# Kernel optimization log

Measured on AMD Instinct MI355X. Metric: run time of the kernel, lower is better.

## Reference

```python
import jax, jax.numpy as jnp
import numpy as np


def setup_inputs() -> dict:
    key = jax.random.key(0)
    x = jax.random.normal(key, (8192, 4096), dtype=jnp.float32)
    return {"x": x, "k": 1}


def reference(x, k):
    # torch.linalg.svdvals returns singular values in descending order;
    # jnp.linalg.svd with compute_uv=False does the same.
    s = jnp.linalg.svd(x, compute_uv=False)  # [min(m, n)], descending
    return jnp.sum(s[:k] ** 2)
```

## Files before the change

kernel.cpp:

```cpp
#include <hip/hip_runtime.h>
#include <hip/hip_fp16.h>
#include <math.h>


#define NROWS 8192
#define NCOLS 4096
#define T_STEPS 16
#define BMV_BLOCKS 512
#define RPC 8

__global__ __launch_bounds__(256) void init_kernel(float* __restrict__ ws) {
    int i = blockIdx.x * 256 + threadIdx.x;
    float* r1 = ws;
    float* r0 = ws + 4096;
    float* slots = ws + 12288;
    unsigned h = (unsigned)i * 2654435761u;
    h ^= h >> 16; h *= 2246822519u; h ^= h >> 13;
    r1[i] = (h & 1u) ? 0.015625f : -0.015625f;
    r0[i] = 0.f;
    if (i < 128) slots[i] = (i == 64 || i == 65) ? 1.f : 0.f;
}

__global__ __launch_bounds__(256) void convert_kernel(const float* __restrict__ A,
                                                      __half* __restrict__ Ah) {
    const float4* A4 = (const float4*)A;
    float2* O2 = (float2*)Ah;
    for (int i = blockIdx.x * 256 + threadIdx.x; i < (NROWS * NCOLS / 4); i += 2048 * 256) {
        float4 f = A4[i];
        union { float2 f2; __half2 h2[2]; } u;
        u.h2[0] = __halves2half2(__float2half_rn(f.x), __float2half_rn(f.y));
        u.h2[1] = __halves2half2(__float2half_rn(f.z), __float2half_rn(f.w));
        O2[i] = u.f2;
    }
}

__device__ __forceinline__ void up8(const float4& p, float* f) {
    const __half2* h = (const __half2*)&p;
    float2 t0 = __half22float2(h[0]);
    float2 t1 = __half22float2(h[1]);
    float2 t2 = __half22float2(h[2]);
    float2 t3 = __half22float2(h[3]);
    f[0] = t0.x; f[1] = t0.y; f[2] = t1.x; f[3] = t1.y;
    f[4] = t2.x; f[5] = t2.y; f[6] = t3.x; f[7] = t3.y;
}

__global__ __launch_bounds__(256, 4) void bmv(const __half* __restrict__ Ah,
                                              const float* __restrict__ rc,
                                              float* __restrict__ partials,
                                              float* __restrict__ slots,
                                              int j) {
    __shared__ float s_lds[RPC];
    int tid = threadIdx.x, lane = tid & 63;
    float inv = rsqrtf(fmaxf(slots[64 + j], 1e-30f));
    int cA = tid * 8, cB = 2048 + tid * 8;
    float vA[8], vB[8];
    {
        const float4* r4 = (const float4*)(rc + cA);
        float4 x = r4[0], y = r4[1];
        vA[0] = x.x * inv; vA[1] = x.y * inv; vA[2] = x.z * inv; vA[3] = x.w * inv;
        vA[4] = y.x * inv; vA[5] = y.y * inv; vA[6] = y.z * inv; vA[7] = y.w * inv;
        const float4* s4 = (const float4*)(rc + cB);
        float4 z = s4[0], w = s4[1];
        vB[0] = z.x * inv; vB[1] = z.y * inv; vB[2] = z.z * inv; vB[3] = z.w * inv;
        vB[4] = w.x * inv; vB[5] = w.y * inv; vB[6] = w.z * inv; vB[7] = w.w * inv;
    }
    float wacc[16];
#pragma unroll
    for (int i = 0; i < 16; ++i) wacc[i] = 0.f;

#pragma unroll 1
    for (int ch = 0; ch < 2; ++ch) {
        int row0 = ch * 4096 + blockIdx.x * RPC;
        const __half* base = Ah + (size_t)row0 * NCOLS;
        float4 alo[RPC], ahi[RPC];
#pragma unroll
        for (int r = 0; r < RPC; ++r) {
            alo[r] = *(const float4*)(base + (size_t)r * NCOLS + cA);
            ahi[r] = *(const float4*)(base + (size_t)r * NCOLS + cB);
        }
        __syncthreads();
        if (tid < RPC) s_lds[tid] = 0.f;
        __syncthreads();
#pragma unroll
        for (int r = 0; r < RPC; ++r) {
            float f[8];
            up8(alo[r], f);
            float sp = f[0] * vA[0] + f[1] * vA[1] + f[2] * vA[2] + f[3] * vA[3]
                     + f[4] * vA[4] + f[5] * vA[5] + f[6] * vA[6] + f[7] * vA[7];
            up8(ahi[r], f);
            sp += f[0] * vB[0] + f[1] * vB[1] + f[2] * vB[2] + f[3] * vB[3]
                + f[4] * vB[4] + f[5] * vB[5] + f[6] * vB[6] + f[7] * vB[7];
#pragma unroll
            for (int off = 32; off > 0; off >>= 1) sp += __shfl_xor(sp, off);
            if (lane == 0) atomicAdd(&s_lds[r], sp);
        }
        __syncthreads();
        if (tid == 0) {
            float aa = 0.f;
#pragma unroll
            for (int r = 0; r < RPC; ++r) aa += s_lds[r] * s_lds[r];
            atomicAdd(&slots[j], aa);
        }
#pragma unroll
        for (int r = 0; r < RPC; ++r) {
            float s = s_lds[r];
            float f[8];
            up8(alo[r], f);
            wacc[0] += s * f[0]; wacc[1] += s * f[1]; wacc[2] += s * f[2]; wacc[3] += s * f[3];
            wacc[4] += s * f[4]; wacc[5] += s * f[5]; wacc[6] += s * f[6]; wacc[7] += s * f[7];
            up8(ahi[r], f);
            wacc[8] += s * f[0]; wacc[9] += s * f[1]; wacc[10] += s * f[2]; wacc[11] += s * f[3];
            wacc[12] += s * f[4]; wacc[13] += s * f[5]; wacc[14] += s * f[6]; wacc[15] += s * f[7];
        }
    }
    float* pb = partials + (size_t)blockIdx.x * NCOLS;
    float4* pa = (float4*)(pb + cA);
    pa[0] = make_float4(wacc[0], wacc[1], wacc[2], wacc[3]);
    pa[1] = make_float4(wacc[4], wacc[5], wacc[6], wacc[7]);
    float4* pc = (float4*)(pb + cB);
    pc[0] = make_float4(wacc[8], wacc[9], wacc[10], wacc[11]);
    pc[1] = make_float4(wacc[12], wacc[13], wacc[14], wacc[15]);
}

__global__ __launch_bounds__(256) void red1(const float* __restrict__ partials,
                                            float* __restrict__ p2) {
    int cb = blockIdx.x >> 5, g = blockIdx.x & 31;
    int col = cb * 256 + threadIdx.x;
    const float* p = partials + (size_t)(g * 16) * NCOLS + col;
    float s = 0.f;
#pragma unroll
    for (int k = 0; k < 16; ++k) s += p[(size_t)k * NCOLS];
    p2[(size_t)g * NCOLS + col] = s;
}

__global__ __launch_bounds__(256) void red2(const float* __restrict__ p2,
                                            float* __restrict__ wt,
                                            const float* __restrict__ rc,
                                            const float* __restrict__ rp,
                                            float* __restrict__ slots,
                                            int j) {
    int tid = threadIdx.x;
    int col = blockIdx.x * 256 + tid;
    float w = 0.f;
#pragma unroll
    for (int g = 0; g < 32; ++g) w += p2[(size_t)g * NCOLS + col];
    float a = slots[j];
    float n2j = fmaxf(slots[64 + j], 1e-30f);
    float n2m = fmaxf(slots[64 + j - 1], 1e-30f);
    float invj = rsqrtf(n2j);
    float cb = sqrtf(n2j / n2m);
    float rn = w - a * invj * rc[col] - cb * rp[col];
    wt[col] = rn;
    float p = rn * rn;
#pragma unroll
    for (int off = 32; off > 0; off >>= 1) p += __shfl_xor(p, off);
    __shared__ float part[4];
    int lane = tid & 63, wq = tid >> 6;
    if (lane == 0) part[wq] = p;
    __syncthreads();
    if (tid == 0)
        atomicAdd(&slots[64 + j + 1], part[0] + part[1] + part[2] + part[3]);
}

__global__ void solve_kernel(const float* __restrict__ slots,
                             float* __restrict__ out, int t) {
    __shared__ float d_s[64], e2_s[64];
    int lane = threadIdx.x;
    d_s[lane] = (lane < t) ? slots[1 + lane] : 0.f;
    e2_s[lane] = (lane < t - 1) ? slots[64 + lane + 2] : 0.f;
    __syncthreads();
    float e_here = sqrtf(e2_s[lane]);
    float e_prev = (lane > 0) ? sqrtf(e2_s[lane - 1]) : 0.f;
    float d = d_s[lane];
    float gersh = (lane < t) ? d + e_here + e_prev : 0.f;
    float dmax = (lane < t) ? d : 0.f;
#pragma unroll
    for (int off = 32; off > 0; off >>= 1) {
        gersh = fmaxf(gersh, __shfl_xor(gersh, off));
        dmax = fmaxf(dmax, __shfl_xor(dmax, off));
    }
    float lo = dmax, hi = gersh + 1e-3f;
    for (int round = 0; round < 3; ++round) {
        float stepw = (hi - lo) * (1.f / 64.f);
        float x = lo + stepw * (lane + 1);
        double qv = 1.0;
        int cnt = 0;
        for (int i = 0; i < t; ++i) {
            double qi = (double)d_s[i] - (double)x - ((i > 0) ? (double)e2_s[i - 1] / qv : 0.0);
            if (fabs(qi) < 1e-300) qi = -1e-300;
            cnt += (qi < 0.0);
            qv = qi;
        }
        unsigned long long m = __ballot(cnt < t);
        if (m) {
            int h = 63 - __clzll(m);
            lo = lo + stepw * (h + 1);
            hi = lo + stepw;
        } else {
            hi = lo + stepw;
        }
    }
    if (lane == 0) out[0] = 0.5f * (lo + hi);
}

extern "C" void kernel_launch(void* const* d_in, const int* in_sizes, int n_in,
                              void* d_out, int out_size, void* d_ws, size_t ws_size,
                              hipStream_t stream) {
    const float* A = (const float*)d_in[0];
    float* out = (float*)d_out;
    float* ws = (float*)d_ws;
    float* vb[3] = {ws, ws + 4096, ws + 8192};
    float* slots = ws + 12288;
    float* p2 = ws + 16384;
    float* partials = ws + 262144;
    __half* Ah = (__half*)((char*)d_ws + (size_t)16 * 1024 * 1024);

    init_kernel<<<16, 256, 0, stream>>>(ws);
    convert_kernel<<<2048, 256, 0, stream>>>(A, Ah);

    const int T = T_STEPS;
    for (int j = 1; j <= T; ++j) {
        float* rc = vb[j % 3];
        float* rp = vb[(j + 2) % 3];
        float* wt = vb[(j + 1) % 3];
        bmv<<<BMV_BLOCKS, 256, 0, stream>>>(Ah, rc, partials, slots, j);
        if (j < T) {
            red1<<<512, 256, 0, stream>>>(partials, p2);
            red2<<<16, 256, 0, stream>>>(p2, wt, rc, rp, slots, j);
        }
    }
    solve_kernel<<<1, 64, 0, stream>>>(slots, out, T);
}
```

Baseline: 848.4 us.

## Fuse Lanczos iterations into one persistent kernel with grid barriers

Replaces the init, convert, per-step matvec, two reduction kernels and the solve kernel with a single persistent kernel of 256 blocks. Stages are separated by atomic-counter grid barriers, and the two-level partial reduction becomes a single in-block reduction per column slice. The goal is to remove dozens of kernel launches and the intermediate reduction buffer. In exchange, it relies on all blocks being co-resident and runs with fewer blocks per matvec. The initial vector placement also changes: the random start vector now sits in the buffer the first step reads.

After: 1.483 ms. 74.8% more time.

```diff
diff --git a/kernel.cpp b/kernel.cpp
--- a/kernel.cpp
+++ b/kernel.cpp
@@ -6,32 +6,25 @@
 #define NROWS 8192
 #define NCOLS 4096
 #define T_STEPS 16
-#define BMV_BLOCKS 512
+#define NBLK 256
 #define RPC 8
-
-__global__ __launch_bounds__(256) void init_kernel(float* __restrict__ ws) {
-    int i = blockIdx.x * 256 + threadIdx.x;
-    float* r1 = ws;
-    float* r0 = ws + 4096;
-    float* slots = ws + 12288;
-    unsigned h = (unsigned)i * 2654435761u;
-    h ^= h >> 16; h *= 2246822519u; h ^= h >> 13;
-    r1[i] = (h & 1u) ? 0.015625f : -0.015625f;
-    r0[i] = 0.f;
-    if (i < 128) slots[i] = (i == 64 || i == 65) ? 1.f : 0.f;
-}
-
-__global__ __launch_bounds__(256) void convert_kernel(const float* __restrict__ A,
-                                                      __half* __restrict__ Ah) {
-    const float4* A4 = (const float4*)A;
-    float2* O2 = (float2*)Ah;
-    for (int i = blockIdx.x * 256 + threadIdx.x; i < (NROWS * NCOLS / 4); i += 2048 * 256) {
-        float4 f = A4[i];
-        union { float2 f2; __half2 h2[2]; } u;
-        u.h2[0] = __halves2half2(__float2half_rn(f.x), __float2half_rn(f.y));
-        u.h2[1] = __halves2half2(__float2half_rn(f.z), __float2half_rn(f.w));
-        O2[i] = u.f2;
-    }
+#define NCHUNK 4
+
+__device__ __forceinline__ float slot_ld(const float* p) {
+    return __hip_atomic_load(p, __ATOMIC_RELAXED, __HIP_MEMORY_SCOPE_AGENT);
+}
+
+__device__ __forceinline__ void gbar(unsigned* cnt) {
+    __syncthreads();
+    if (threadIdx.x == 0) {
+        __threadfence();
+        __hip_atomic_fetch_add(cnt, 1u, __ATOMIC_ACQ_REL, __HIP_MEMORY_SCOPE_AGENT);
+        while (__hip_atomic_load(cnt, __ATOMIC_ACQUIRE, __HIP_MEMORY_SCOPE_AGENT) < NBLK) {
+            __builtin_amdgcn_s_sleep(2);
+        }
+        __threadfence();
+    }
+    __syncthreads();
 }
 
 __device__ __forceinline__ void up8(const float4& p, float* f) {
@@ -44,163 +37,206 @@
     f[4] = t2.x; f[5] = t2.y; f[6] = t3.x; f[7] = t3.y;
 }
 
-__global__ __launch_bounds__(256, 4) void bmv(const __half* __restrict__ Ah,
-                                              const float* __restrict__ rc,
-                                              float* __restrict__ partials,
-                                              float* __restrict__ slots,
-                                              int j) {
-    __shared__ float s_lds[RPC];
-    int tid = threadIdx.x, lane = tid & 63;
-    float inv = rsqrtf(fmaxf(slots[64 + j], 1e-30f));
-    int cA = tid * 8, cB = 2048 + tid * 8;
-    float vA[8], vB[8];
+__global__ __launch_bounds__(256, 2) void lanczos_fused(const float* __restrict__ A,
+                                                        __half* __restrict__ Ah,
+                                                        float* __restrict__ ws,
+                                                        float* __restrict__ out) {
+    __shared__ __align__(16) float smem[192];
+    float* slots = ws + 12288;
+    unsigned* bars = (unsigned*)(ws + 12416);
+    float* partials = ws + 262144;
+    const int tid = threadIdx.x;
+    const int bid = blockIdx.x;
+    const int gtid = bid * 256 + tid;
+    int bix = 0;
+
     {
-        const float4* r4 = (const float4*)(rc + cA);
-        float4 x = r4[0], y = r4[1];
-        vA[0] = x.x * inv; vA[1] = x.y * inv; vA[2] = x.z * inv; vA[3] = x.w * inv;
-        vA[4] = y.x * inv; vA[5] = y.y * inv; vA[6] = y.z * inv; vA[7] = y.w * inv;
-        const float4* s4 = (const float4*)(rc + cB);
-        float4 z = s4[0], w = s4[1];
-        vB[0] = z.x * inv; vB[1] = z.y * inv; vB[2] = z.z * inv; vB[3] = z.w * inv;
-        vB[4] = w.x * inv; vB[5] = w.y * inv; vB[6] = w.z * inv; vB[7] = w.w * inv;
-    }
-    float wacc[16];
-#pragma unroll
-    for (int i = 0; i < 16; ++i) wacc[i] = 0.f;
+        const float4* A4 = (const float4*)A;
+        float2* O2 = (float2*)Ah;
+#pragma unroll 4
+        for (int i = gtid; i < (NROWS * NCOLS / 4); i += NBLK * 256) {
+            float4 f = A4[i];
+            union { float2 f2; __half2 h2[2]; } u;
+            u.h2[0] = __halves2half2(__float2half_rn(f.x), __float2half_rn(f.y));
+            u.h2[1] = __halves2half2(__float2half_rn(f.z), __float2half_rn(f.w));
+            O2[i] = u.f2;
+        }
+        if (gtid < NCOLS) {
+            unsigned h = (unsigned)gtid * 2654435761u;
+            h ^= h >> 16; h *= 2246822519u; h ^= h >> 13;
+            ws[4096 + gtid] = (h & 1u) ? 0.015625f : -0.015625f;
+            ws[gtid] = 0.f;
+            if (gtid < 128) slots[gtid] = (gtid == 64 || gtid == 65) ? 1.f : 0.f;
+        }
+    }
+    gbar(&bars[bix++]);
+
+    for (int j = 1; j <= T_STEPS; ++j) {
+        const float* rc = ws + 4096 * (j % 3);
+        const float* rp = ws + 4096 * ((j + 2) % 3);
+        float* wt = ws + 4096 * ((j + 1) % 3);
+
+        {
+            int lane = tid & 63;
+            float inv = rsqrtf(fmaxf(slot_ld(&slots[64 + j]), 1e-30f));
+            int cA = tid * 8, cB = 2048 + tid * 8;
+            float vA[8], vB[8];
+            {
+                const float4* r4 = (const float4*)(rc + cA);
+                float4 x = r4[0], y = r4[1];
+                vA[0] = x.x * inv; vA[1] = x.y * inv; vA[2] = x.z * inv; vA[3] = x.w * inv;
+                vA[4] = y.x * inv; vA[5] = y.y * inv; vA[6] = y.z * inv; vA[7] = y.w * inv;
+                const float4* s4 = (const float4*)(rc + cB);
+                float4 z = s4[0], w4 = s4[1];
+                vB[0] = z.x * inv; vB[1] = z.y * inv; vB[2] = z.z * inv; vB[3] = z.w * inv;
+                vB[4] = w4.x * inv; vB[5] = w4.y * inv; vB[6] = w4.z * inv; vB[7] = w4.w * inv;
+            }
+            float wacc[16];
+#pragma unroll
+            for (int i = 0; i < 16; ++i) wacc[i] = 0.f;
 
 #pragma unroll 1
-    for (int ch = 0; ch < 2; ++ch) {
-        int row0 = ch * 4096 + blockIdx.x * RPC;
-        const __half* base = Ah + (size_t)row0 * NCOLS;
-        float4 alo[RPC], ahi[RPC];
-#pragma unroll
-        for (int r = 0; r < RPC; ++r) {
-            alo[r] = *(const float4*)(base + (size_t)r * NCOLS + cA);
-            ahi[r] = *(const float4*)(base + (size_t)r * NCOLS + cB);
+            for (int ch = 0; ch < NCHUNK; ++ch) {
+                int row0 = ch * (NBLK * RPC) + bid * RPC;
+                const __half* base = Ah + (size_t)row0 * NCOLS;
+                float4 alo[RPC], ahi[RPC];
+#pragma unroll
+                for (int r = 0; r < RPC; ++r) {
+                    alo[r] = *(const float4*)(base + (size_t)r * NCOLS + cA);
+                    ahi[r] = *(const float4*)(base + (size_t)r * NCOLS + cB);
+                }
+                __syncthreads();
+                if (tid < RPC) smem[tid] = 0.f;
+                __syncthreads();
+#pragma unroll
+                for (int r = 0; r < RPC; ++r) {
+                    float f[8];
+                    up8(alo[r], f);
+                    float sp = f[0] * vA[0] + f[1] * vA[1] + f[2] * vA[2] + f[3] * vA[3]
+                             + f[4] * vA[4] + f[5] * vA[5] + f[6] * vA[6] + f[7] * vA[7];
+                    up8(ahi[r], f);
+                    sp += f[0] * vB[0] + f[1] * vB[1] + f[2] * vB[2] + f[3] * vB[3]
+                        + f[4] * vB[4] + f[5] * vB[5] + f[6] * vB[6] + f[7] * vB[7];
+#pragma unroll
+                    for (int off = 32; off > 0; off >>= 1) sp += __shfl_xor(sp, off);
+                    if (lane == 0) atomicAdd(&smem[r], sp);
+                }
+                __syncthreads();
+                if (tid == 0) {
+                    float aa = 0.f;
+#pragma unroll
+                    for (int r = 0; r < RPC; ++r) aa += smem[r] * smem[r];
+                    atomicAdd(&slots[j], aa);
+                }
+#pragma unroll
+                for (int r = 0; r < RPC; ++r) {
+                    float s = smem[r];
+                    float f[8];
+                    up8(alo[r], f);
+                    wacc[0] += s * f[0]; wacc[1] += s * f[1]; wacc[2] += s * f[2]; wacc[3] += s * f[3];
+                    wacc[4] += s * f[4]; wacc[5] += s * f[5]; wacc[6] += s * f[6]; wacc[7] += s * f[7];
+                    up8(ahi[r], f);
+                    wacc[8] += s * f[0]; wacc[9] += s * f[1]; wacc[10] += s * f[2]; wacc[11] += s * f[3];
+                    wacc[12] += s * f[4]; wacc[13] += s * f[5]; wacc[14] += s * f[6]; wacc[15] += s * f[7];
+                }
+            }
+            float* pb = partials + (size_t)bid * NCOLS;
+            float4* pa = (float4*)(pb + cA);
+            pa[0] = make_float4(wacc[0], wacc[1], wacc[2], wacc[3]);
+            pa[1] = make_float4(wacc[4], wacc[5], wacc[6], wacc[7]);
+            float4* pc = (float4*)(pb + cB);
+            pc[0] = make_float4(wacc[8], wacc[9], wacc[10], wacc[11]);
+            pc[1] = make_float4(wacc[12], wacc[13], wacc[14], wacc[15]);
+        }
+        gbar(&bars[bix++]);
+
+        if (j < T_STEPS) {
+            {
+                int q = tid & 3, p0 = tid >> 2;
+                float4 s = make_float4(0.f, 0.f, 0.f, 0.f);
+#pragma unroll
+                for (int i = 0; i < 4; ++i) {
+                    const float4 v = *(const float4*)(partials
+                        + (size_t)(p0 + i * 64) * NCOLS + bid * 16 + q * 4);
+                    s.x += v.x; s.y += v.y; s.z += v.z; s.w += v.w;
+                }
+#pragma unroll
+                for (int off = 4; off <= 32; off <<= 1) {
+                    s.x += __shfl_xor(s.x, off);
+                    s.y += __shfl_xor(s.y, off);
+                    s.z += __shfl_xor(s.z, off);
+                    s.w += __shfl_xor(s.w, off);
+                }
+                int lane = tid & 63, wv = tid >> 6;
+                if (lane < 4) *(float4*)&smem[wv * 16 + lane * 4] = s;
+                __syncthreads();
+                if (tid < 16) {
+                    int col = bid * 16 + tid;
+                    float wsum = smem[tid] + smem[16 + tid] + smem[32 + tid] + smem[48 + tid];
+                    float a = slot_ld(&slots[j]);
+                    float n2j = fmaxf(slot_ld(&slots[64 + j]), 1e-30f);
+                    float n2m = fmaxf(slot_ld(&slots[64 + j - 1]), 1e-30f);
+                    float invj = rsqrtf(n2j);
+                    float cb = sqrtf(n2j / n2m);
+                    float rn = wsum - a * invj * rc[col] - cb * rp[col];
+                    wt[col] = rn;
+                    float p = rn * rn;
+                    p += __shfl_xor(p, 1);
+                    p += __shfl_xor(p, 2);
+                    p += __shfl_xor(p, 4);
+                    p += __shfl_xor(p, 8);
+                    if (tid == 0) atomicAdd(&slots[64 + j + 1], p);
+                }
+            }
+            gbar(&bars[bix++]);
+        }
+    }
+
+    if (bid == 0) {
+        const int t = T_STEPS;
+        float* d_s = smem;
+        float* e2_s = smem + 64;
+        if (tid < 64) {
+            d_s[tid] = (tid < t) ? slot_ld(&slots[1 + tid]) : 0.f;
+            e2_s[tid] = (tid < t - 1) ? slot_ld(&slots[64 + tid + 2]) : 0.f;
         }
         __syncthreads();
-        if (tid < RPC) s_lds[tid] = 0.f;
-        __syncthreads();
-#pragma unroll
-        for (int r = 0; r < RPC; ++r) {
-            float f[8];
-            up8(alo[r], f);
-            float sp = f[0] * vA[0] + f[1] * vA[1] + f[2] * vA[2] + f[3] * vA[3]
-                     + f[4] * vA[4] + f[5] * vA[5] + f[6] * vA[6] + f[7] * vA[7];
-            up8(ahi[r], f);
-            sp += f[0] * vB[0] + f[1] * vB[1] + f[2] * vB[2] + f[3] * vB[3]
-                + f[4] * vB[4] + f[5] * vB[5] + f[6] * vB[6] + f[7] * vB[7];
-#pragma unroll
-            for (int off = 32; off > 0; off >>= 1) sp += __shfl_xor(sp, off);
-            if (lane == 0) atomicAdd(&s_lds[r], sp);
-        }
-        __syncthreads();
-        if (tid == 0) {
-            float aa = 0.f;
-#pragma unroll
-            for (int r = 0; r < RPC; ++r) aa += s_lds[r] * s_lds[r];
-            atomicAdd(&slots[j], aa);
-        }
-#pragma unroll
-        for (int r = 0; r < RPC; ++r) {
-            float s = s_lds[r];
-            float f[8];
-            up8(alo[r], f);
-            wacc[0] += s * f[0]; wacc[1] += s * f[1]; wacc[2] += s * f[2]; wacc[3] += s * f[3];
-            wacc[4] += s * f[4]; wacc[5] += s * f[5]; wacc[6] += s * f[6]; wacc[7] += s * f[7];
-            up8(ahi[r], f);
-            wacc[8] += s * f[0]; wacc[9] += s * f[1]; wacc[10] += s * f[2]; wacc[11] += s * f[3];
-            wacc[12] += s * f[4]; wacc[13] += s * f[5]; wacc[14] += s * f[6]; wacc[15] += s * f[7];
-        }
-    }
-    float* pb = partials + (size_t)blockIdx.x * NCOLS;
-    float4* pa = (float4*)(pb + cA);
-    pa[0] = make_float4(wacc[0], wacc[1], wacc[2], wacc[3]);
-    pa[1] = make_float4(wacc[4], wacc[5], wacc[6], wacc[7]);
-    float4* pc = (float4*)(pb + cB);
-    pc[0] = make_float4(wacc[8], wacc[9], wacc[10], wacc[11]);
-    pc[1] = make_float4(wacc[12], wacc[13], wacc[14], wacc[15]);
-}
-
-__global__ __launch_bounds__(256) void red1(const float* __restrict__ partials,
-                                            float* __restrict__ p2) {
-    int cb = blockIdx.x >> 5, g = blockIdx.x & 31;
-    int col = cb * 256 + threadIdx.x;
-    const float* p = partials + (size_t)(g * 16) * NCOLS + col;
-    float s = 0.f;
-#pragma unroll
-    for (int k = 0; k < 16; ++k) s += p[(size_t)k * NCOLS];
-    p2[(size_t)g * NCOLS + col] = s;
-}
-
-__global__ __launch_bounds__(256) void red2(const float* __restrict__ p2,
-                                            float* __restrict__ wt,
-                                            const float* __restrict__ rc,
-                                            const float* __restrict__ rp,
-                                            float* __restrict__ slots,
-                                            int j) {
-    int tid = threadIdx.x;
-    int col = blockIdx.x * 256 + tid;
-    float w = 0.f;
-#pragma unroll
-    for (int g = 0; g < 32; ++g) w += p2[(size_t)g * NCOLS + col];
-    float a = slots[j];
-    float n2j = fmaxf(slots[64 + j], 1e-30f);
-    float n2m = fmaxf(slots[64 + j - 1], 1e-30f);
-    float invj = rsqrtf(n2j);
-    float cb = sqrtf(n2j / n2m);
-    float rn = w - a * invj * rc[col] - cb * rp[col];
-    wt[col] = rn;
-    float p = rn * rn;
-#pragma unroll
-    for (int off = 32; off > 0; off >>= 1) p += __shfl_xor(p, off);
-    __shared__ float part[4];
-    int lane = tid & 63, wq = tid >> 6;
-    if (lane == 0) part[wq] = p;
-    __syncthreads();
-    if (tid == 0)
-        atomicAdd(&slots[64 + j + 1], part[0] + part[1] + part[2] + part[3]);
-}
-
-__global__ void solve_kernel(const float* __restrict__ slots,
-                             float* __restrict__ out, int t) {
-    __shared__ float d_s[64], e2_s[64];
-    int lane = threadIdx.x;
-    d_s[lane] = (lane < t) ? slots[1 + lane] : 0.f;
-    e2_s[lane] = (lane < t - 1) ? slots[64 + lane + 2] : 0.f;
-    __syncthreads();
-    float e_here = sqrtf(e2_s[lane]);
-    float e_prev = (lane > 0) ? sqrtf(e2_s[lane - 1]) : 0.f;
-    float d = d_s[lane];
-    float gersh = (lane < t) ? d + e_here + e_prev : 0.f;
-    float dmax = (lane < t) ? d : 0.f;
-#pragma unroll
-    for (int off = 32; off > 0; off >>= 1) {
-        gersh = fmaxf(gersh, __shfl_xor(gersh, off));
-        dmax = fmaxf(dmax, __shfl_xor(dmax, off));
-    }
-    float lo = dmax, hi = gersh + 1e-3f;
-    for (int round = 0; round < 3; ++round) {
-        float stepw = (hi - lo) * (1.f / 64.f);
-        float x = lo + stepw * (lane + 1);
-        double qv = 1.0;
-        int cnt = 0;
-        for (int i = 0; i < t; ++i) {
-            double qi = (double)d_s[i] - (double)x - ((i > 0) ? (double)e2_s[i - 1] / qv : 0.0);
-            if (fabs(qi) < 1e-300) qi = -1e-300;
-            cnt += (qi < 0.0);
-            qv = qi;
-        }
-        unsigned long long m = __ballot(cnt < t);
-        if (m) {
-            int h = 63 - __clzll(m);
-            lo = lo + stepw * (h + 1);
-            hi = lo + stepw;
-        } else {
-            hi = lo + stepw;
-        }
-    }
-    if (lane == 0) out[0] = 0.5f * (lo + hi);
+        if (tid < 64) {
+            int lane = tid;
+            float e_here = sqrtf(e2_s[lane]);
+            float e_prev = (lane > 0) ? sqrtf(e2_s[lane - 1]) : 0.f;
+            float d = d_s[lane];
+            float gersh = (lane < t) ? d + e_here + e_prev : 0.f;
+            float dmax = (lane < t) ? d : 0.f;
+#pragma unroll
+            for (int off = 32; off > 0; off >>= 1) {
+                gersh = fmaxf(gersh, __shfl_xor(gersh, off));
+                dmax = fmaxf(dmax, __shfl_xor(dmax, off));
+            }
+            float lo = dmax, hi = gersh + 1e-3f;
+            for (int round = 0; round < 3; ++round) {
+                float stepw = (hi - lo) * (1.f / 64.f);
+                float x = lo + stepw * (lane + 1);
+                double qv = 1.0;
+                int cnt = 0;
+                for (int i = 0; i < t; ++i) {
+                    double qi = (double)d_s[i] - (double)x - ((i > 0) ? (double)e2_s[i - 1] / qv : 0.0);
+                    if (fabs(qi) < 1e-300) qi = -1e-300;
+                    cnt += (qi < 0.0);
+                    qv = qi;
+                }
+                unsigned long long m = __ballot(cnt < t);
+                if (m) {
+                    int h = 63 - __clzll(m);
+                    lo = lo + stepw * (h + 1);
+                    hi = lo + stepw;
+                } else {
+                    hi = lo + stepw;
+                }
+            }
+            if (tid == 0) out[0] = 0.5f * (lo + hi);
+        }
+    }
 }
 
 extern "C" void kernel_launch(void* const* d_in, const int* in_sizes, int n_in,
@@ -209,25 +245,9 @@
     const float* A = (const float*)d_in[0];
     float* out = (float*)d_out;
     float* ws = (float*)d_ws;
-    float* vb[3] = {ws, ws + 4096, ws + 8192};
-    float* slots = ws + 12288;
-    float* p2 = ws + 16384;
-    float* partials = ws + 262144;
     __half* Ah = (__half*)((char*)d_ws + (size_t)16 * 1024 * 1024);
 
-    init_kernel<<<16, 256, 0, stream>>>(ws);
-    convert_kernel<<<2048, 256, 0, stream>>>(A, Ah);
-
-    const int T = T_STEPS;
-    for (int j = 1; j <= T; ++j) {
-        float* rc = vb[j % 3];
-        float* rp = vb[(j + 2) % 3];
-        float* wt = vb[(j + 1) % 3];
-        bmv<<<BMV_BLOCKS, 256, 0, stream>>>(Ah, rc, partials, slots, j);
-        if (j < T) {
-            red1<<<512, 256, 0, stream>>>(partials, p2);
-            red2<<<16, 256, 0, stream>>>(p2, wt, rc, rp, slots, j);
-        }
-    }
-    solve_kernel<<<1, 64, 0, stream>>>(slots, out, T);
-}
+    hipMemsetAsync((char*)d_ws + (size_t)12416 * 4, 0, 64 * sizeof(unsigned), stream);
+
+    lanczos_fused<<<NBLK, 256, 0, stream>>>(A, Ah, ws, out);
+}
```
